# Optimization experiments

Measured on AMD Instinct MI355X. Metric: run time of the kernel, lower is better.

Reference implementation:

```python
import jax, jax.numpy as jnp
import numpy as np

N_NODES = 100000
N_EDGES = 3200000
IN_FEAT = 128
HIDDEN = 32
NUM_LAYERS = 4
K = 35
NODES_PER_GRAPH = 100


def setup_inputs() -> dict:
    key = jax.random.key(0)
    ks = jax.random.split(key, 20)
    inp = {}
    inp['x'] = jax.random.normal(ks[0], (N_NODES, IN_FEAT), dtype=jnp.float32)
    inp['edge_index'] = jax.random.randint(ks[1], (2, N_EDGES), 0, N_NODES, dtype=jnp.int64)
    inp['batch'] = (jnp.arange(N_NODES, dtype=jnp.int64) // NODES_PER_GRAPH)
    # GCNConv weights (PyG: lin weight [in, out], bias [out])
    dims = [IN_FEAT] + [HIDDEN] * NUM_LAYERS
    for i in range(NUM_LAYERS):
        s = 1.0 / np.sqrt(dims[i])
        inp[f'w{i}'] = jax.random.normal(ks[2 + i], (dims[i], HIDDEN), dtype=jnp.float32) * s
        inp[f'b{i}'] = jnp.zeros((HIDDEN,), dtype=jnp.float32)
    # head: Conv1d(128->16,k=1), Conv1d(16->32,k=5), fc1(416->128), fc2(128->1)
    inp['conv1_w'] = jax.random.normal(ks[8], (16, HIDDEN * NUM_LAYERS, 1), dtype=jnp.float32) * (1.0 / np.sqrt(128))
    inp['conv1_b'] = jnp.zeros((16,), dtype=jnp.float32)
    inp['conv2_w'] = jax.random.normal(ks[9], (32, 16, 5), dtype=jnp.float32) * (1.0 / np.sqrt(16 * 5))
    inp['conv2_b'] = jnp.zeros((32,), dtype=jnp.float32)
    lin_in = 32 * (K // 2 - 4)  # 416
    inp['fc1_w'] = jax.random.normal(ks[10], (128, lin_in), dtype=jnp.float32) * (1.0 / np.sqrt(lin_in))
    inp['fc1_b'] = jnp.zeros((128,), dtype=jnp.float32)
    inp['fc2_w'] = jax.random.normal(ks[11], (1, 128), dtype=jnp.float32) * (1.0 / np.sqrt(128))
    inp['fc2_b'] = jnp.zeros((1,), dtype=jnp.float32)
    return inp


def _gcn_conv(x, w, b, src, dst, n):
    # PyG GCNConv: h = x @ W; add self-loops; sym-normalized scatter-add; + bias
    h = x @ w
    deg = jnp.ones((n,), h.dtype).at[dst].add(1.0)  # degree incl. self-loop
    dis = jax.lax.rsqrt(deg)
    coef = dis[src] * dis[dst]  # [E]
    agg = jax.ops.segment_sum(h[src] * coef[:, None], dst, num_segments=n)
    return agg + h / deg[:, None] + b  # self-loop norm = 1/deg


def reference(x, edge_index, batch, w0, b0, w1, b1, w2, b2, w3, b3,
              conv1_w, conv1_b, conv2_w, conv2_b, fc1_w, fc1_b, fc2_w, fc2_b):
    src, dst = edge_index[0], edge_index[1]
    n = x.shape[0]
    xs = []
    h = x
    for w, b in ((w0, b0), (w1, b1), (w2, b2), (w3, b3)):
        h = jnp.tanh(_gcn_conv(h, w, b, src, dst, n))
        xs.append(h)
    feat = jnp.concatenate(xs, axis=1)  # [N, 128]
    # global_sort_pool: graphs are contiguous blocks of NODES_PER_GRAPH nodes
    G = n // NODES_PER_GRAPH
    dense = feat.reshape(G, NODES_PER_GRAPH, -1)
    order = jnp.argsort(-dense[:, :, -1], axis=1)  # descending by last channel
    topk = jnp.take_along_axis(dense, order[:, :, None], axis=1)[:, :K]  # [G,K,128]
    y = topk.transpose(0, 2, 1)  # [G,128,K]
    y = jax.nn.relu(jnp.einsum('oc,gck->gok', conv1_w[:, :, 0], y) + conv1_b[None, :, None])
    L = y.shape[-1] // 2  # MaxPool1d(2), drop trailing element
    y = y[..., :L * 2].reshape(G, 16, L, 2).max(axis=-1)  # [G,16,17]
    y = jax.lax.conv_general_dilated(y, conv2_w, (1,), 'VALID',
                                     dimension_numbers=('NCH', 'OIH', 'NCH'))
    y = jax.nn.relu(y + conv2_b[None, :, None])  # [G,32,13]
    y = y.reshape(G, -1)  # [G,416]
    y = jax.nn.relu(y @ fc1_w.T + fc1_b)  # dropout is identity in eval
    return jax.nn.sigmoid(y @ fc2_w.T + fc2_b)  # [G,1]
```

## Files before the change

kernel.cpp:

```cpp
#include <hip/hip_runtime.h>
#include <hip/hip_fp16.h>
#include <math.h>

#define N_NODES 100000
#define N_EDGES 3200000
#define HIDDEN 32
#define K_TOP 35
#define NPG 100
#define N_GRAPHS 1000

#define BSHIFT 9
#define NLOC 512
#define NBUCK 196
#define CAP 17408
#define NBB 1024
#define BIN_CHUNK 13


__global__ void k_bin(const int* __restrict__ src, const int* __restrict__ dst,
                      int* __restrict__ bcnt, unsigned int* __restrict__ bdata) {
    __shared__ int h[NBUCK];
    __shared__ int lbase[NBUCK];
    __shared__ int lcur[NBUCK];
    int t = threadIdx.x;
    for (int i = t; i < NBUCK; i += 256) { h[i] = 0; lcur[i] = 0; }
    __syncthreads();
    int base = blockIdx.x * (256 * BIN_CHUNK);
    int ss[BIN_CHUNK], ds[BIN_CHUNK];
#pragma unroll
    for (int k = 0; k < BIN_CHUNK; k++) {
        int e = base + k * 256 + t;
        if (e < N_EDGES) {
            ss[k] = src[e];
            ds[k] = dst[e];
            atomicAdd(&h[ds[k] >> BSHIFT], 1);
        } else ds[k] = -1;
    }
    __syncthreads();
    for (int i = t; i < NBUCK; i += 256)
        lbase[i] = h[i] ? atomicAdd(&bcnt[i], h[i]) : 0;
    __syncthreads();
#pragma unroll
    for (int k = 0; k < BIN_CHUNK; k++) {
        int d = ds[k];
        if (d >= 0) {
            int bk = d >> BSHIFT;
            int pos = atomicAdd(&lcur[bk], 1);
            bdata[bk * CAP + lbase[bk] + pos] =
                ((unsigned int)ss[k] << BSHIFT) | (unsigned int)(d & (NLOC - 1));
        }
    }
}

__global__ void k_build(const unsigned int* __restrict__ bdata, const int* __restrict__ bcnt,
                        int2* __restrict__ rc, float* __restrict__ dis,
                        int* __restrict__ csr) {
    __shared__ int h[NLOC];
    __shared__ int sd[NLOC];
    __shared__ int rp[NLOC];
    __shared__ int cur[NLOC];
    int b = blockIdx.x, t = threadIdx.x;
    if (t < NLOC) h[t] = 0;
    __syncthreads();
    int r0 = b * CAP, r1 = r0 + bcnt[b];
    for (int i = r0 + t; i < r1; i += 1024)
        atomicAdd(&h[bdata[i] & (NLOC - 1)], 1);
    __syncthreads();
    int v = (t < NLOC) ? h[t] : 0;
    if (t < NLOC) sd[t] = v;
    __syncthreads();
    for (int off = 1; off < NLOC; off <<= 1) {
        int x = (t >= off && t < NLOC) ? sd[t - off] : 0;
        __syncthreads();
        if (t < NLOC) sd[t] += x;
        __syncthreads();
    }
    if (t < NLOC) {
        int excl = sd[t] - v;
        int node = (b << BSHIFT) + t;
        rp[t] = r0 + excl;
        cur[t] = 0;
        if (node < N_NODES) {
            rc[node] = make_int2(r0 + excl, v);
            dis[node] = rsqrtf((float)(v + 1));
        }
    }
    __syncthreads();
    for (int i = r0 + t; i < r1; i += 1024) {
        unsigned int u = bdata[i];
        int loc = u & (NLOC - 1);
        int pos = atomicAdd(&cur[loc], 1);
        csr[rp[loc] + pos] = (int)(u >> BSHIFT);
    }
}


__global__ void k_mm0(const float* __restrict__ in, const float* __restrict__ w,
                      const float* __restrict__ dis, char* __restrict__ hs) {
    __shared__ float wl[128 * HIDDEN];
    int t = threadIdx.x;
    for (int i = t; i < 128 * HIDDEN; i += 256) wl[i] = w[i];
    __syncthreads();
    int n0 = blockIdx.x * 512 + t;
    int n1 = n0 + 256;
    bool has0 = n0 < N_NODES, has1 = n1 < N_NODES;
    int m0 = has0 ? n0 : 0, m1 = has1 ? n1 : 0;
    const float* r0p = in + (size_t)m0 * 128;
    const float* r1p = in + (size_t)m1 * 128;
    float acc0[HIDDEN], acc1[HIDDEN];
#pragma unroll
    for (int o = 0; o < HIDDEN; o++) { acc0[o] = 0.f; acc1[o] = 0.f; }
    for (int c4 = 0; c4 < 32; c4++) {
        float4 va = *(const float4*)(r0p + c4 * 4);
        float4 vb = *(const float4*)(r1p + c4 * 4);
        float xa[4] = {va.x, va.y, va.z, va.w};
        float xb[4] = {vb.x, vb.y, vb.z, vb.w};
#pragma unroll
        for (int k = 0; k < 4; k++) {
            const float* wr = &wl[(c4 * 4 + k) * HIDDEN];
#pragma unroll
            for (int o = 0; o < HIDDEN; o++) {
                float wv = wr[o];
                acc0[o] += xa[k] * wv;
                acc1[o] += xb[k] * wv;
            }
        }
    }
    if (has0) {
        float d = dis[m0];
        float4* hr = (float4*)(hs + (size_t)m0 * 64);
#pragma unroll
        for (int qq = 0; qq < 4; qq++) {
            __half2 p[4];
#pragma unroll
            for (int k = 0; k < 4; k++)
                p[k] = __floats2half2_rn(acc0[8 * qq + 2 * k] * d, acc0[8 * qq + 2 * k + 1] * d);
            hr[qq] = *(float4*)p;
        }
    }
    if (has1) {
        float d = dis[m1];
        float4* hr = (float4*)(hs + (size_t)m1 * 64);
#pragma unroll
        for (int qq = 0; qq < 4; qq++) {
            __half2 p[4];
#pragma unroll
            for (int k = 0; k < 4; k++)
                p[k] = __floats2half2_rn(acc1[8 * qq + 2 * k] * d, acc1[8 * qq + 2 * k + 1] * d);
            hr[qq] = *(float4*)p;
        }
    }
}

__global__ void k_agg(const float4* __restrict__ hs4, const float* __restrict__ dis,
                      const int2* __restrict__ rc, const int* __restrict__ csr_src,
                      const float* __restrict__ bias,
                      float* __restrict__ feat, int col_off,
                      const float* __restrict__ wnext, char* __restrict__ hsn) {
    __shared__ float wl[32 * 33];
    __shared__ float tv[4][36];
    int tt = threadIdx.x;
    if (wnext) {
        for (int i = tt; i < 1024; i += 256)
            wl[(i >> 5) * 33 + (i & 31)] = wnext[i];
    }
    __syncthreads();
    int n = (blockIdx.x * 256 + tt) >> 6;
    int c = tt & 63;
    int r = c & 3;
    int ph = c >> 2;
    int p7 = ph & 7;
    int slot = tt >> 6;
    int2 rcv = rc[n];
    int start = rcv.x, m = rcv.y;
    float d = dis[n];
    float4 sv = hs4[(size_t)n * 4 + r];
    float acc[8] = {0.f, 0.f, 0.f, 0.f, 0.f, 0.f, 0.f, 0.f};

    for (int base = 0; base < m; base += 64) {
        int e = base + c;
        int idx = (e < m) ? csr_src[start + e] : N_NODES;
        int id0 = __shfl(idx, ph, 64);
        int id1 = __shfl(idx, 16 + ph, 64);
        int id2 = __shfl(idx, 32 + ph, 64);
        int id3 = __shfl(idx, 48 + ph, 64);
        float4 g0 = hs4[(size_t)id0 * 4 + r];
        float4 g1 = hs4[(size_t)id1 * 4 + r];
        float4 g2 = hs4[(size_t)id2 * 4 + r];
        float4 g3 = hs4[(size_t)id3 * 4 + r];
        const __half2* h0 = (const __half2*)&g0;
        const __half2* h1 = (const __half2*)&g1;
        const __half2* h2 = (const __half2*)&g2;
        const __half2* h3 = (const __half2*)&g3;
        float2 f;
#pragma unroll
        for (int j = 0; j < 4; j++) {
            f = __half22float2(h0[j]); acc[2 * j] += f.x; acc[2 * j + 1] += f.y;
        }
#pragma unroll
        for (int j = 0; j < 4; j++) {
            f = __half22float2(h1[j]); acc[2 * j] += f.x; acc[2 * j + 1] += f.y;
        }
#pragma unroll
        for (int j = 0; j < 4; j++) {
            f = __half22float2(h2[j]); acc[2 * j] += f.x; acc[2 * j + 1] += f.y;
        }
#pragma unroll
        for (int j = 0; j < 4; j++) {
            f = __half22float2(h3[j]); acc[2 * j] += f.x; acc[2 * j + 1] += f.y;
        }
    }
    float s[8];
#pragma unroll
    for (int k = 0; k < 8; k++) {
        float v = acc[k];
        v += __shfl_xor(v, 4);
        v += __shfl_xor(v, 8);
        v += __shfl_xor(v, 16);
        v += __shfl_xor(v, 32);
        s[k] = v;
    }
    float s01 = (p7 & 1) ? s[1] : s[0];
    float s23 = (p7 & 1) ? s[3] : s[2];
    float s45 = (p7 & 1) ? s[5] : s[4];
    float s67 = (p7 & 1) ? s[7] : s[6];
    float s03 = (p7 & 2) ? s23 : s01;
    float s47 = (p7 & 2) ? s67 : s45;
    float sp  = (p7 & 4) ? s47 : s03;
    const __half2* sh = (const __half2*)&sv;
    __half2 q01 = (p7 & 2) ? sh[1] : sh[0];
    __half2 q23 = (p7 & 2) ? sh[3] : sh[2];
    __half2 qq  = (p7 & 4) ? q23 : q01;
    float self = (p7 & 1) ? __high2float(qq) : __low2float(qq);
    float bv = bias[8 * r + p7];
    float ov = tanhf(d * (sp + self) + bv);
    if (ph < 8)
        __builtin_nontemporal_store(ov, &feat[(size_t)n * 128 + col_off + 8 * r + p7]);
    if (wnext) {
        if (ph < 8) tv[slot][8 * r + p7] = ov;
        __builtin_amdgcn_wave_barrier();
        int cc = c & 31;
        int kbase = (c >> 5) * 16;
        float o = 0.f;
#pragma unroll 8
        for (int k2 = 0; k2 < 16; k2++)
            o += tv[slot][kbase + k2] * wl[(kbase + k2) * 33 + cc];
        o += __shfl_xor(o, 32);
        o *= d;
        float oh = __shfl_xor(o, 1);
        if (c < 32 && (c & 1) == 0) {
            __half2 pck = __floats2half2_rn(o, oh);
            *(__half2*)(hsn + (size_t)n * 64 + (size_t)cc * 2) = pck;
        }
    }
}


__global__ void __launch_bounds__(256, 4)
k_head(const float* __restrict__ feat,
       const float* __restrict__ c1w, const float* __restrict__ c1b,
       const float* __restrict__ c2w, const float* __restrict__ c2b,
       const float* __restrict__ f1w, const float* __restrict__ f1b,
       const float* __restrict__ f2w, const float* __restrict__ f2b,
       float* __restrict__ out) {
    __shared__ float vals[NPG];
    __shared__ int sel[K_TOP];
    __shared__ float tk[K_TOP * 132];
    __shared__ float wl1[16 * 129];
    __shared__ float y1[16][36];
    __shared__ float y2[16][17];
    __shared__ float y3[416];
    __shared__ float y4[128];
    __shared__ float r2[128];
    int g = blockIdx.x, t = threadIdx.x;
    const float* fg = feat + (size_t)g * NPG * 128;

    for (int i = t; i < 2048; i += 256)
        wl1[(i >> 7) * 129 + (i & 127)] = c1w[i];
    if (t < NPG) vals[t] = fg[t * 128 + 127];
    __syncthreads();
    if (t < NPG) {
        float v = vals[t];
        int r = 0;
        for (int j = 0; j < NPG; j++) {
            float u = vals[j];
            r += (u > v) || (u == v && j < t);
        }
        if (r < K_TOP) sel[r] = t;
    }
    __syncthreads();
    for (int i = t; i < K_TOP * 32; i += 256) {
        int k = i >> 5, c4 = i & 31;
        *(float4*)&tk[k * 132 + 4 * c4] = *(const float4*)&fg[sel[k] * 128 + 4 * c4];
    }
    __syncthreads();
    for (int i = t; i < 16 * K_TOP; i += 256) {
        int o = i & 15, k = i >> 4;
        float s = c1b[o];
        const float* wr = &wl1[o * 129];
        const float* xr = &tk[k * 132];
#pragma unroll 8
        for (int c = 0; c < 128; c++) s += wr[c] * xr[c];
        y1[o][k] = fmaxf(s, 0.f);
    }
    __syncthreads();
    for (int i = t; i < 16 * 17; i += 256) {
        int o = i & 15, l = i >> 4;
        y2[o][l] = fmaxf(y1[o][2 * l], y1[o][2 * l + 1]);
    }
    __syncthreads();
    for (int idx = t; idx < 32 * 13; idx += 256) {
        int o2 = idx / 13, ttp = idx - o2 * 13;
        float s = c2b[o2];
        const float* wr = c2w + o2 * 80;
#pragma unroll
        for (int i = 0; i < 16; i++)
#pragma unroll
            for (int j = 0; j < 5; j++) s += wr[i * 5 + j] * y2[i][ttp + j];
        y3[idx] = fmaxf(s, 0.f);
    }
    __syncthreads();
    {
        int o = t >> 1, h = t & 1;
        const float4* wr4 = (const float4*)(f1w + o * 416) + h * 52;
        const float* yb = y3 + h * 208;
        float s = 0.f;
#pragma unroll 4
        for (int i = 0; i < 52; i++) {
            float4 w4 = wr4[i];
            s += w4.x * yb[4 * i] + w4.y * yb[4 * i + 1] +
                 w4.z * yb[4 * i + 2] + w4.w * yb[4 * i + 3];
        }
        s += __shfl_xor(s, 1);
        if (h == 0) y4[o] = fmaxf(s + f1b[o], 0.f);
    }
    __syncthreads();
    if (t < 128) r2[t] = f2w[t] * y4[t];
    __syncthreads();
    for (int off = 64; off > 0; off >>= 1) {
        if (t < off) r2[t] += r2[t + off];
        __syncthreads();
    }
    if (t == 0) out[g] = 1.0f / (1.0f + expf(-(r2[0] + f2b[0])));
}


static inline size_t alignup(size_t x) { return (x + 255) & ~(size_t)255; }

extern "C" void kernel_launch(void* const* d_in, const int* in_sizes, int n_in,
                              void* d_out, int out_size, void* d_ws, size_t ws_size,
                              hipStream_t stream) {
    const float* x    = (const float*)d_in[0];
    const int*   ei   = (const int*)d_in[1];
    const int*   srcp = ei;
    const int*   dstp = ei + N_EDGES;
    const float* w0 = (const float*)d_in[3];
    const float* b0 = (const float*)d_in[4];
    const float* w1 = (const float*)d_in[5];
    const float* b1 = (const float*)d_in[6];
    const float* w2 = (const float*)d_in[7];
    const float* b2 = (const float*)d_in[8];
    const float* w3 = (const float*)d_in[9];
    const float* b3 = (const float*)d_in[10];
    const float* c1w = (const float*)d_in[11];
    const float* c1b = (const float*)d_in[12];
    const float* c2w = (const float*)d_in[13];
    const float* c2b = (const float*)d_in[14];
    const float* f1w = (const float*)d_in[15];
    const float* f1b = (const float*)d_in[16];
    const float* f2w = (const float*)d_in[17];
    const float* f2b = (const float*)d_in[18];
    float* out = (float*)d_out;

    char* p = (char*)d_ws;
    int2* rcv    = (int2*)p; p += alignup(sizeof(int2) * N_NODES);
    float* dis   = (float*)p; p += alignup(sizeof(float) * N_NODES);
    int* bcnt    = (int*)p; p += alignup(sizeof(int) * NBUCK);
    int* csr     = (int*)p; p += alignup(sizeof(int) * (size_t)NBUCK * CAP);
    char* U = p;
    unsigned int* bdata = (unsigned int*)U;
    char* hsA = U;
    char* hsB = U + alignup((size_t)N_NODES * 64 + 64);
    size_t usz = alignup(sizeof(unsigned int) * (size_t)NBUCK * CAP);
    float* feat = (float*)(U + usz);

    const int NB_M = (N_NODES + 511) / 512;
    const int NB_A = (N_NODES * 64) / 256;

    hipMemsetAsync(bcnt, 0, sizeof(int) * NBUCK, stream);
    k_bin<<<NBB, 256, 0, stream>>>(srcp, dstp, bcnt, bdata);
    k_build<<<NBUCK, 1024, 0, stream>>>(bdata, bcnt, rcv, dis, csr);

    hipMemsetAsync(hsA + (size_t)N_NODES * 64, 0, 64, stream);
    hipMemsetAsync(hsB + (size_t)N_NODES * 64, 0, 64, stream);

    k_mm0<<<NB_M, 256, 0, stream>>>(x, w0, dis, hsA);
    k_agg<<<NB_A, 256, 0, stream>>>((const float4*)hsA, dis, rcv, csr, b0,
                                    feat, 0, w1, hsB);
    k_agg<<<NB_A, 256, 0, stream>>>((const float4*)hsB, dis, rcv, csr, b1,
                                    feat, 32, w2, hsA);
    k_agg<<<NB_A, 256, 0, stream>>>((const float4*)hsA, dis, rcv, csr, b2,
                                    feat, 64, w3, hsB);
    k_agg<<<NB_A, 256, 0, stream>>>((const float4*)hsB, dis, rcv, csr, b3,
                                    feat, 96, (const float*)nullptr, (char*)nullptr);

    k_head<<<N_GRAPHS, 256, 0, stream>>>(feat, c1w, c1b, c2w, c2b,
                                         f1w, f1b, f2w, f2b, out);
}
```

Measured before the change: 480.9 us.

## Use 32 lanes per node in GCN aggregation instead of a full wavefront

The aggregation kernel now assigns 32 threads (half a wave64) to each destination node instead of 64. Each iteration gathers 32 edges, with two split accumulators and nontemporal loads of the CSR indices. This removes the idle lanes in the epilogue (previously only 32 of 64 produced output) and the extra shuffle stage, and halves the grid. The risk is less memory-level parallelism per node: average degree is about 32, so each node needs about one loop iteration either way, and half-wave shuffles may be less efficient.

```diff
diff --git a/kernel.cpp b/kernel.cpp
--- a/kernel.cpp
+++ b/kernel.cpp
@@ -158,32 +158,32 @@
                       float* __restrict__ feat, int col_off,
                       const float* __restrict__ wnext, char* __restrict__ hsn) {
     __shared__ float wl[32 * 33];
-    __shared__ float tv[4][36];
+    __shared__ float tv[8][36];
     int tt = threadIdx.x;
     if (wnext) {
         for (int i = tt; i < 1024; i += 256)
             wl[(i >> 5) * 33 + (i & 31)] = wnext[i];
     }
     __syncthreads();
-    int n = (blockIdx.x * 256 + tt) >> 6;
-    int c = tt & 63;
+    int n = (blockIdx.x * 256 + tt) >> 5;
+    int c = tt & 31;
     int r = c & 3;
     int ph = c >> 2;
-    int p7 = ph & 7;
-    int slot = tt >> 6;
+    int slot = tt >> 5;
     int2 rcv = rc[n];
     int start = rcv.x, m = rcv.y;
     float d = dis[n];
     float4 sv = hs4[(size_t)n * 4 + r];
-    float acc[8] = {0.f, 0.f, 0.f, 0.f, 0.f, 0.f, 0.f, 0.f};
-
-    for (int base = 0; base < m; base += 64) {
+    float aA[8] = {0.f, 0.f, 0.f, 0.f, 0.f, 0.f, 0.f, 0.f};
+    float aB[8] = {0.f, 0.f, 0.f, 0.f, 0.f, 0.f, 0.f, 0.f};
+
+    for (int base = 0; base < m; base += 32) {
         int e = base + c;
-        int idx = (e < m) ? csr_src[start + e] : N_NODES;
-        int id0 = __shfl(idx, ph, 64);
-        int id1 = __shfl(idx, 16 + ph, 64);
-        int id2 = __shfl(idx, 32 + ph, 64);
-        int id3 = __shfl(idx, 48 + ph, 64);
+        int idx = (e < m) ? __builtin_nontemporal_load(csr_src + start + e) : N_NODES;
+        int id0 = __shfl(idx, ph, 32);
+        int id1 = __shfl(idx, 8 + ph, 32);
+        int id2 = __shfl(idx, 16 + ph, 32);
+        int id3 = __shfl(idx, 24 + ph, 32);
         float4 g0 = hs4[(size_t)id0 * 4 + r];
         float4 g1 = hs4[(size_t)id1 * 4 + r];
         float4 g2 = hs4[(size_t)id2 * 4 + r];
@@ -195,62 +195,57 @@
         float2 f;
 #pragma unroll
         for (int j = 0; j < 4; j++) {
-            f = __half22float2(h0[j]); acc[2 * j] += f.x; acc[2 * j + 1] += f.y;
+            f = __half22float2(h0[j]); aA[2 * j] += f.x; aA[2 * j + 1] += f.y;
         }
 #pragma unroll
         for (int j = 0; j < 4; j++) {
-            f = __half22float2(h1[j]); acc[2 * j] += f.x; acc[2 * j + 1] += f.y;
+            f = __half22float2(h1[j]); aB[2 * j] += f.x; aB[2 * j + 1] += f.y;
         }
 #pragma unroll
         for (int j = 0; j < 4; j++) {
-            f = __half22float2(h2[j]); acc[2 * j] += f.x; acc[2 * j + 1] += f.y;
+            f = __half22float2(h2[j]); aA[2 * j] += f.x; aA[2 * j + 1] += f.y;
         }
 #pragma unroll
         for (int j = 0; j < 4; j++) {
-            f = __half22float2(h3[j]); acc[2 * j] += f.x; acc[2 * j + 1] += f.y;
+            f = __half22float2(h3[j]); aB[2 * j] += f.x; aB[2 * j + 1] += f.y;
         }
     }
     float s[8];
 #pragma unroll
     for (int k = 0; k < 8; k++) {
-        float v = acc[k];
+        float v = aA[k] + aB[k];
         v += __shfl_xor(v, 4);
         v += __shfl_xor(v, 8);
         v += __shfl_xor(v, 16);
-        v += __shfl_xor(v, 32);
         s[k] = v;
     }
-    float s01 = (p7 & 1) ? s[1] : s[0];
-    float s23 = (p7 & 1) ? s[3] : s[2];
-    float s45 = (p7 & 1) ? s[5] : s[4];
-    float s67 = (p7 & 1) ? s[7] : s[6];
-    float s03 = (p7 & 2) ? s23 : s01;
-    float s47 = (p7 & 2) ? s67 : s45;
-    float sp  = (p7 & 4) ? s47 : s03;
+    float s01 = (ph & 1) ? s[1] : s[0];
+    float s23 = (ph & 1) ? s[3] : s[2];
+    float s45 = (ph & 1) ? s[5] : s[4];
+    float s67 = (ph & 1) ? s[7] : s[6];
+    float s03 = (ph & 2) ? s23 : s01;
+    float s47 = (ph & 2) ? s67 : s45;
+    float sp  = (ph & 4) ? s47 : s03;
     const __half2* sh = (const __half2*)&sv;
-    __half2 q01 = (p7 & 2) ? sh[1] : sh[0];
-    __half2 q23 = (p7 & 2) ? sh[3] : sh[2];
-    __half2 qq  = (p7 & 4) ? q23 : q01;
-    float self = (p7 & 1) ? __high2float(qq) : __low2float(qq);
-    float bv = bias[8 * r + p7];
+    __half2 q01 = (ph & 2) ? sh[1] : sh[0];
+    __half2 q23 = (ph & 2) ? sh[3] : sh[2];
+    __half2 qq  = (ph & 4) ? q23 : q01;
+    float self = (ph & 1) ? __high2float(qq) : __low2float(qq);
+    float bv = bias[8 * r + ph];
     float ov = tanhf(d * (sp + self) + bv);
-    if (ph < 8)
-        __builtin_nontemporal_store(ov, &feat[(size_t)n * 128 + col_off + 8 * r + p7]);
+    __builtin_nontemporal_store(ov, &feat[(size_t)n * 128 + col_off + 8 * r + ph]);
     if (wnext) {
-        if (ph < 8) tv[slot][8 * r + p7] = ov;
+        tv[slot][8 * r + ph] = ov;
         __builtin_amdgcn_wave_barrier();
-        int cc = c & 31;
-        int kbase = (c >> 5) * 16;
         float o = 0.f;
 #pragma unroll 8
-        for (int k2 = 0; k2 < 16; k2++)
-            o += tv[slot][kbase + k2] * wl[(kbase + k2) * 33 + cc];
-        o += __shfl_xor(o, 32);
+        for (int k = 0; k < 32; k++)
+            o += tv[slot][k] * wl[k * 33 + c];
         o *= d;
         float oh = __shfl_xor(o, 1);
-        if (c < 32 && (c & 1) == 0) {
+        if ((c & 1) == 0) {
             __half2 pck = __floats2half2_rn(o, oh);
-            *(__half2*)(hsn + (size_t)n * 64 + (size_t)cc * 2) = pck;
+            *(__half2*)(hsn + (size_t)n * 64 + (size_t)c * 2) = pck;
         }
     }
 }
@@ -385,7 +380,7 @@
     float* feat = (float*)(U + usz);
 
     const int NB_M = (N_NODES + 511) / 512;
-    const int NB_A = (N_NODES * 64) / 256;
+    const int NB_A = (N_NODES * 32) / 256;
 
     hipMemsetAsync(bcnt, 0, sizeof(int) * NBUCK, stream);
     k_bin<<<NBB, 256, 0, stream>>>(srcp, dstp, bcnt, bdata);
```

After: 446.1 us. -7.2%, faster.
